# Kernel optimization log

Hardware: AMD Instinct MI355X
Metric: run time of the kernel (lower is better)

Reference implementation:

```python
import jax, jax.numpy as jnp
import numpy as np

N_CHARS = 256
EMB = 1024
HID = 2048
SEQ = 8192

def setup_inputs() -> dict:
    key = jax.random.key(0)
    ks = jax.random.split(key, 7)
    s = 0.02
    return {
        "input_seq": jax.random.randint(ks[0], (SEQ,), 0, N_CHARS),
        "emb": jax.random.normal(ks[1], (N_CHARS, EMB), jnp.float32) * s,
        "wax_w": jax.random.normal(ks[2], (HID, EMB), jnp.float32) * s,
        "wax_b": jnp.zeros((HID,), jnp.float32),
        "waa_w": jax.random.normal(ks[3], (HID, HID), jnp.float32) * s,
        "wya_w": jax.random.normal(ks[4], (N_CHARS, HID), jnp.float32) * s,
        "wya_b": jnp.zeros((N_CHARS,), jnp.float32),
    }

def reference(input_seq, emb, wax_w, wax_b, waa_w, wya_w, wya_b):
    # Embed whole sequence: [T, E]
    x_seq = emb[input_seq]
    # Precompute the input projection for all steps (parallel GEMM): [T, H]
    xa_seq = x_seq @ wax_w.T + wax_b

    def step(h, xa):
        h_new = jnp.tanh(xa + h @ waa_w.T)  # [H]
        o = h_new @ wya_w.T + wya_b          # [n_chars]
        return h_new, o

    h0 = jnp.zeros((HID,), x_seq.dtype)
    h_final, out = jax.lax.scan(step, h0, xa_seq)
    # out: [T, n_chars]; hidden returned as [1, H] to match torch module
    return out, h_final[None, :]
```

## Files before the change

### kernel.cpp

```cpp
#include <hip/hip_runtime.h>
#include <stdint.h>

#define SEQ 8192
#define EMB 1024
#define HID 2048
#define NCH 256

#define SCAN_B 64
#define SCAN_T 512
#define ROWS_PB (HID / SCAN_B)
#define SENT 0xFFFFFFFFu
#define NREP 4
#define NSLOT 8

typedef unsigned uint4v __attribute__((ext_vector_type(4)));
typedef unsigned long long u64;

__global__ __launch_bounds__(256) void gemm_tn(const float* __restrict__ X,
                                               const float* __restrict__ W,
                                               const float* __restrict__ bias,
                                               float* __restrict__ C,
                                               int M, int N, int K)
{
    __shared__ float Xs[16][68];
    __shared__ float Ws[16][68];
    const int m0 = blockIdx.x * 64, n0 = blockIdx.y * 64;
    const int tid  = threadIdx.x;
    const int lrow = tid >> 2;
    const int kq   = (tid & 3) * 4;
    const int tx   = tid & 15, ty = tid >> 4;
    float acc[4][4] = {};
    const float* Xp = X + (size_t)(m0 + lrow) * K + kq;
    const float* Wp = W + (size_t)(n0 + lrow) * K + kq;

    for (int k0 = 0; k0 < K; k0 += 16) {
        float4 xv = *(const float4*)(Xp + k0);
        float4 wv = *(const float4*)(Wp + k0);
        __syncthreads();
        Xs[kq+0][lrow] = xv.x; Xs[kq+1][lrow] = xv.y;
        Xs[kq+2][lrow] = xv.z; Xs[kq+3][lrow] = xv.w;
        Ws[kq+0][lrow] = wv.x; Ws[kq+1][lrow] = wv.y;
        Ws[kq+2][lrow] = wv.z; Ws[kq+3][lrow] = wv.w;
        __syncthreads();
#pragma unroll
        for (int kk = 0; kk < 16; ++kk) {
            float4 av = *(const float4*)&Xs[kk][ty * 4];
            float4 bv = *(const float4*)&Ws[kk][tx * 4];
            float a[4] = {av.x, av.y, av.z, av.w};
            float b[4] = {bv.x, bv.y, bv.z, bv.w};
#pragma unroll
            for (int i = 0; i < 4; ++i)
#pragma unroll
                for (int j = 0; j < 4; ++j)
                    acc[i][j] += a[i] * b[j];
        }
    }
#pragma unroll
    for (int i = 0; i < 4; ++i) {
        const int m = m0 + ty * 4 + i;
#pragma unroll
        for (int j = 0; j < 4; ++j) {
            const int n = n0 + tx * 4 + j;
            C[(size_t)m * N + n] = acc[i][j] + bias[n];
        }
    }
}

__device__ __forceinline__ float fast_tanh(float x)
{
    float e = __builtin_amdgcn_exp2f(x * 2.885390081777927f);
    return 1.0f - 2.0f * __builtin_amdgcn_rcpf(e + 1.0f);
}

__device__ __forceinline__ u64 ld_agent(const u64* p)
{
    return __hip_atomic_load(p, __ATOMIC_RELAXED, __HIP_MEMORY_SCOPE_AGENT);
}

__device__ __forceinline__ int is_poison(u64 x0, u64 x1)
{
    return ((unsigned)x0 == SENT) | ((unsigned)(x0 >> 32) == SENT) |
           ((unsigned)x1 == SENT) | ((unsigned)(x1 >> 32) == SENT);
}

__global__ __launch_bounds__(SCAN_T, 2) void rnn_scan(
    const int*  __restrict__ seq,
    const float* __restrict__ waa,
    const float* __restrict__ P,
    float* __restrict__ H,
    unsigned* __restrict__ ring)
{
    const int b    = blockIdx.x;
    const int tid  = threadIdx.x;
    const int wv   = tid >> 6;
    const int lane = tid & 63;
    const int R0   = b * ROWS_PB + wv * 4;
    const int rep  = b & (NREP - 1);

    __shared__ float hbuf[2][HID];
    __shared__ int   flg[2][8];

    float w0[32], w1[32], w2[32], w3[32];
#pragma unroll
    for (int j = 0; j < 8; ++j) {
        const float* base = waa + 256 * j + 4 * lane;
        float4 a = *(const float4*)(base + (size_t)(R0 + 0) * HID);
        float4 c = *(const float4*)(base + (size_t)(R0 + 1) * HID);
        float4 d = *(const float4*)(base + (size_t)(R0 + 2) * HID);
        float4 e = *(const float4*)(base + (size_t)(R0 + 3) * HID);
        w0[4*j+0]=a.x; w0[4*j+1]=a.y; w0[4*j+2]=a.z; w0[4*j+3]=a.w;
        w1[4*j+0]=c.x; w1[4*j+1]=c.y; w1[4*j+2]=c.z; w1[4*j+3]=c.w;
        w2[4*j+0]=d.x; w2[4*j+1]=d.y; w2[4*j+2]=d.z; w2[4*j+3]=d.w;
        w3[4*j+0]=e.x; w3[4*j+1]=e.y; w3[4*j+2]=e.z; w3[4*j+3]=e.w;
    }
#pragma unroll
    for (int k = 0; k < 32; ++k) {
        asm volatile("" : "+v"(w0[k])); asm volatile("" : "+v"(w1[k]));
        asm volatile("" : "+v"(w2[k])); asm volatile("" : "+v"(w3[k]));
    }

    if (tid < 16) ((int*)flg)[tid] = -1;
    __syncthreads();

    unsigned* myring = ring + (size_t)rep * NSLOT * HID;

#pragma unroll 1
    for (int t = 0; t < SEQ; ++t) {
        const int ch = seq[t];
        float xav = 0.f;
        if (lane < 4) xav = P[(size_t)ch * HID + R0 + lane];

        u64 x0, x1;
        {
            const u64* p8 = (const u64*)
                (myring + (size_t)(t & (NSLOT - 1)) * HID + tid * 4);
            u64 a0 = ld_agent(p8 + 0), a1 = ld_agent(p8 + 1);
            u64 b0 = ld_agent(p8 + 0), b1 = ld_agent(p8 + 1);
            u64 c0 = ld_agent(p8 + 0), c1 = ld_agent(p8 + 1);
            for (;;) {
                if (!is_poison(a0, a1)) { x0 = a0; x1 = a1; break; }
                a0 = ld_agent(p8 + 0); a1 = ld_agent(p8 + 1);
                if (!is_poison(b0, b1)) { x0 = b0; x1 = b1; break; }
                b0 = ld_agent(p8 + 0); b1 = ld_agent(p8 + 1);
                if (!is_poison(c0, c1)) { x0 = c0; x1 = c1; break; }
                c0 = ld_agent(p8 + 0); c1 = ld_agent(p8 + 1);
            }
        }
        uint4v v;
        v.x = (unsigned)x0; v.y = (unsigned)(x0 >> 32);
        v.z = (unsigned)x1; v.w = (unsigned)(x1 >> 32);
        *(uint4v*)&hbuf[t & 1][tid * 4] = v;

        asm volatile("s_waitcnt lgkmcnt(0)" ::: "memory");
        if (lane == 0) *(volatile int*)&flg[t & 1][wv] = t;

        float a0 = 0.f, a1 = 0.f, a2 = 0.f, a3 = 0.f;
        const float* hb = &hbuf[t & 1][4 * lane];
#pragma unroll
        for (int j = 0; j < 8; ++j) {
            while (*(volatile int*)&flg[t & 1][j] != t) { }
            asm volatile("" ::: "memory");
            float4 hv = *(const float4*)(hb + 256 * j);
            a0 += w0[4*j+0]*hv.x + w0[4*j+1]*hv.y + w0[4*j+2]*hv.z + w0[4*j+3]*hv.w;
            a1 += w1[4*j+0]*hv.x + w1[4*j+1]*hv.y + w1[4*j+2]*hv.z + w1[4*j+3]*hv.w;
            a2 += w2[4*j+0]*hv.x + w2[4*j+1]*hv.y + w2[4*j+2]*hv.z + w2[4*j+3]*hv.w;
            a3 += w3[4*j+0]*hv.x + w3[4*j+1]*hv.y + w3[4*j+2]*hv.z + w3[4*j+3]*hv.w;
        }

        __builtin_amdgcn_s_setprio(1);

        a0 += __shfl_xor(a0, 1, 64);
        a1 += __shfl_xor(a1, 1, 64);
        a2 += __shfl_xor(a2, 1, 64);
        a3 += __shfl_xor(a3, 1, 64);
        float m01 = (lane & 1) ? a1 : a0;
        float m23 = (lane & 1) ? a3 : a2;
        m01 += __shfl_xor(m01, 2, 64);
        m23 += __shfl_xor(m23, 2, 64);
        float m = (lane & 2) ? m23 : m01;
        m += __shfl_xor(m, 4, 64);
        m += __shfl_xor(m, 8, 64);
        m += __shfl_xor(m, 16, 64);
        m += __shfl_xor(m, 32, 64);

        if (lane < 4) {
            float hn = fast_tanh(xav + m);
            const unsigned hu = __float_as_uint(hn);
            const int row = R0 + lane;
            const int s1 = (t + 1) & (NSLOT - 1);
            const int s5 = (t + 5) & (NSLOT - 1);
#pragma unroll
            for (int r = 0; r < NREP; ++r)
                __hip_atomic_store(ring + ((size_t)r * NSLOT + s1) * HID + row,
                                   hu, __ATOMIC_RELAXED,
                                   __HIP_MEMORY_SCOPE_AGENT);
#pragma unroll
            for (int r = 0; r < NREP; ++r)
                __hip_atomic_store(ring + ((size_t)r * NSLOT + s5) * HID + row,
                                   SENT, __ATOMIC_RELAXED,
                                   __HIP_MEMORY_SCOPE_AGENT);
            H[(size_t)(t + 1) * HID + row] = hn;
        }
        __builtin_amdgcn_s_setprio(0);
    }
}

__global__ void copy_h(const float* __restrict__ src, float* __restrict__ dst)
{
    int i = blockIdx.x * blockDim.x + threadIdx.x;
    if (i < HID) dst[i] = src[i];
}

extern "C" void kernel_launch(void* const* d_in, const int* in_sizes, int n_in,
                              void* d_out, int out_size, void* d_ws, size_t ws_size,
                              hipStream_t stream)
{
    const int*   seq  = (const int*)  d_in[0];
    const float* emb  = (const float*)d_in[1];
    const float* wax  = (const float*)d_in[2];
    const float* waxb = (const float*)d_in[3];
    const float* waa  = (const float*)d_in[4];
    const float* wya  = (const float*)d_in[5];
    const float* wyab = (const float*)d_in[6];
    float* out = (float*)d_out;

    float*    H    = (float*)d_ws;
    float*    P    = (float*)((char*)d_ws + (size_t)(SEQ + 1) * HID * sizeof(float));
    unsigned* ring = (unsigned*)(P + (size_t)NCH * HID);

    (void)hipMemsetAsync(ring, 0xFF, (size_t)NREP * NSLOT * HID * sizeof(unsigned), stream);
    for (int r = 0; r < NREP; ++r)
        (void)hipMemsetAsync(ring + (size_t)r * NSLOT * HID, 0,
                             HID * sizeof(unsigned), stream);

    dim3 gA(NCH / 64, HID / 64);
    gemm_tn<<<gA, 256, 0, stream>>>(emb, wax, waxb, P, NCH, HID, EMB);

    rnn_scan<<<SCAN_B, SCAN_T, 0, stream>>>(seq, waa, P, H, ring);

    dim3 gC(SEQ / 64, NCH / 64);
    gemm_tn<<<gC, 256, 0, stream>>>(H + HID, wya, wyab, out, SEQ, NCH, HID);

    copy_h<<<(HID + 255) / 256, 256, 0, stream>>>(H + (size_t)SEQ * HID,
                                                  out + (size_t)SEQ * NCH);
}
```

Before: 17.20 ms.

## Read recurrent state directly from global ring per wave, drop LDS staging

Each wave now loads the full hidden vector straight from its own replica of the global ring buffer, which grows from four to eight replicas and is indexed by wave instead of block. This removes the LDS staging buffer, the per-wave LDS flags and the intra-block spin-waits. Each wave polls its own slices for the poison sentinel and accumulates as soon as a slice is ready. In exchange, every wave issues eight times more global loads per step, and each producer writes eight replicas per row. The s_setprio hints are also removed.

```diff
diff --git a/kernel.cpp b/kernel.cpp
--- a/kernel.cpp
+++ b/kernel.cpp
@@ -10,10 +10,9 @@
 #define SCAN_T 512
 #define ROWS_PB (HID / SCAN_B)
 #define SENT 0xFFFFFFFFu
-#define NREP 4
+#define NREP 8
 #define NSLOT 8
 
-typedef unsigned uint4v __attribute__((ext_vector_type(4)));
 typedef unsigned long long u64;
 
 __global__ __launch_bounds__(256) void gemm_tn(const float* __restrict__ X,
@@ -95,10 +94,6 @@
     const int wv   = tid >> 6;
     const int lane = tid & 63;
     const int R0   = b * ROWS_PB + wv * 4;
-    const int rep  = b & (NREP - 1);
-
-    __shared__ float hbuf[2][HID];
-    __shared__ int   flg[2][8];
 
     float w0[32], w1[32], w2[32], w3[32];
 #pragma unroll
@@ -119,10 +114,7 @@
         asm volatile("" : "+v"(w2[k])); asm volatile("" : "+v"(w3[k]));
     }
 
-    if (tid < 16) ((int*)flg)[tid] = -1;
-    __syncthreads();
-
-    unsigned* myring = ring + (size_t)rep * NSLOT * HID;
+    unsigned* myring = ring + (size_t)wv * NSLOT * HID;
 
 #pragma unroll 1
     for (int t = 0; t < SEQ; ++t) {
@@ -130,44 +122,33 @@
         float xav = 0.f;
         if (lane < 4) xav = P[(size_t)ch * HID + R0 + lane];
 
-        u64 x0, x1;
-        {
-            const u64* p8 = (const u64*)
-                (myring + (size_t)(t & (NSLOT - 1)) * HID + tid * 4);
-            u64 a0 = ld_agent(p8 + 0), a1 = ld_agent(p8 + 1);
-            u64 b0 = ld_agent(p8 + 0), b1 = ld_agent(p8 + 1);
-            u64 c0 = ld_agent(p8 + 0), c1 = ld_agent(p8 + 1);
-            for (;;) {
-                if (!is_poison(a0, a1)) { x0 = a0; x1 = a1; break; }
-                a0 = ld_agent(p8 + 0); a1 = ld_agent(p8 + 1);
-                if (!is_poison(b0, b1)) { x0 = b0; x1 = b1; break; }
-                b0 = ld_agent(p8 + 0); b1 = ld_agent(p8 + 1);
-                if (!is_poison(c0, c1)) { x0 = c0; x1 = c1; break; }
-                c0 = ld_agent(p8 + 0); c1 = ld_agent(p8 + 1);
+        const u64* p8 = (const u64*)
+            (myring + (size_t)(t & (NSLOT - 1)) * HID) + 2 * lane;
+
+        u64 lo[8], hi[8];
+#pragma unroll
+        for (int j = 0; j < 8; ++j) {
+            lo[j] = ld_agent(p8 + 128 * j);
+            hi[j] = ld_agent(p8 + 128 * j + 1);
+        }
+
+        float a0 = 0.f, a1 = 0.f, a2 = 0.f, a3 = 0.f;
+#pragma unroll
+        for (int j = 0; j < 8; ++j) {
+            u64 x0 = lo[j], x1 = hi[j];
+            while (is_poison(x0, x1)) {
+                x0 = ld_agent(p8 + 128 * j);
+                x1 = ld_agent(p8 + 128 * j + 1);
             }
-        }
-        uint4v v;
-        v.x = (unsigned)x0; v.y = (unsigned)(x0 >> 32);
-        v.z = (unsigned)x1; v.w = (unsigned)(x1 >> 32);
-        *(uint4v*)&hbuf[t & 1][tid * 4] = v;
-
-        asm volatile("s_waitcnt lgkmcnt(0)" ::: "memory");
-        if (lane == 0) *(volatile int*)&flg[t & 1][wv] = t;
-
-        float a0 = 0.f, a1 = 0.f, a2 = 0.f, a3 = 0.f;
-        const float* hb = &hbuf[t & 1][4 * lane];
-#pragma unroll
-        for (int j = 0; j < 8; ++j) {
-            while (*(volatile int*)&flg[t & 1][j] != t) { }
-            asm volatile("" ::: "memory");
-            float4 hv = *(const float4*)(hb + 256 * j);
-            a0 += w0[4*j+0]*hv.x + w0[4*j+1]*hv.y + w0[4*j+2]*hv.z + w0[4*j+3]*hv.w;
-            a1 += w1[4*j+0]*hv.x + w1[4*j+1]*hv.y + w1[4*j+2]*hv.z + w1[4*j+3]*hv.w;
-            a2 += w2[4*j+0]*hv.x + w2[4*j+1]*hv.y + w2[4*j+2]*hv.z + w2[4*j+3]*hv.w;
-            a3 += w3[4*j+0]*hv.x + w3[4*j+1]*hv.y + w3[4*j+2]*hv.z + w3[4*j+3]*hv.w;
-        }
-
-        __builtin_amdgcn_s_setprio(1);
+            const float h0 = __uint_as_float((unsigned)(x0));
+            const float h1 = __uint_as_float((unsigned)(x0 >> 32));
+            const float h2 = __uint_as_float((unsigned)(x1));
+            const float h3 = __uint_as_float((unsigned)(x1 >> 32));
+            a0 += w0[4*j+0]*h0 + w0[4*j+1]*h1 + w0[4*j+2]*h2 + w0[4*j+3]*h3;
+            a1 += w1[4*j+0]*h0 + w1[4*j+1]*h1 + w1[4*j+2]*h2 + w1[4*j+3]*h3;
+            a2 += w2[4*j+0]*h0 + w2[4*j+1]*h1 + w2[4*j+2]*h2 + w2[4*j+3]*h3;
+            a3 += w3[4*j+0]*h0 + w3[4*j+1]*h1 + w3[4*j+2]*h2 + w3[4*j+3]*h3;
+        }
 
         a0 += __shfl_xor(a0, 1, 64);
         a1 += __shfl_xor(a1, 1, 64);
@@ -201,7 +182,6 @@
                                    __HIP_MEMORY_SCOPE_AGENT);
             H[(size_t)(t + 1) * HID + row] = hn;
         }
-        __builtin_amdgcn_s_setprio(0);
     }
 }
 
```

New measurement: 54.94 ms. 219% more time.
